# Kernel tuning notes

Hardware: AMD Instinct MI355X
Metric: run time of the kernel (lower is better)

## Reference

```python
import jax, jax.numpy as jnp
import numpy as np

B, L, QD, H, D = 2, 2048, 1024, 16, 64  # batch, seq, q_dim, heads, head_dim
INNER = H * D


def rms_norm(x, scale):
    # matches torch RMSNorm: mean over last dim in fp32, eps=1e-6, learned scale
    rrms = jax.lax.rsqrt(jnp.mean(x.astype(jnp.float32) ** 2, axis=-1, keepdims=True) + 1e-6)
    return (x * rrms).astype(x.dtype) * scale


def apply_rope(xq, xk, pe):
    # pe: [1,1,L,D//2,2,2] rotation-matrix pairs (FLUX-style)
    def rot(x):
        xs = x.reshape(*x.shape[:-1], D // 2, 1, 2)  # B H L D/2 1 2
        out = pe[..., 0] * xs[..., 0] + pe[..., 1] * xs[..., 1]  # B H L D/2 2
        return out.reshape(x.shape).astype(x.dtype)
    return rot(xq), rot(xk)


def setup_inputs() -> dict:
    key = jax.random.key(0)
    ks = jax.random.split(key, 6)
    s = 0.02
    return {
        "x": jax.random.normal(ks[0], (B, L, QD), jnp.float32),
        "pe": jax.random.normal(ks[1], (1, 1, L, D // 2, 2, 2), jnp.float32),
        "Wq": jax.random.normal(ks[2], (INNER, QD), jnp.float32) * s,
        "Wkv": jax.random.normal(ks[3], (2 * INNER, QD), jnp.float32) * s,
        "Wproj": jax.random.normal(ks[4], (QD, INNER), jnp.float32) * s,
        "bproj": jnp.zeros((QD,), jnp.float32),
        "q_scale": jnp.ones((D,), jnp.float32),
        "k_scale": jnp.ones((D,), jnp.float32),
    }


def reference(x, pe, Wq, Wkv, Wproj, bproj, q_scale, k_scale):
    # q/kv projections (self-attention: context = x)
    q = jnp.einsum('blc,ec->ble', x, Wq).reshape(B, L, H, D).transpose(0, 2, 1, 3)  # B H L D
    kv = jnp.einsum('blc,ec->ble', x, Wkv).reshape(B, L, 2, H, D)  # layout (K H D)
    k = kv[:, :, 0].transpose(0, 2, 1, 3)  # B H L D
    v = kv[:, :, 1].transpose(0, 2, 1, 3)  # B H L D
    # per-head QK RMSNorm
    q = rms_norm(q, q_scale)
    k = rms_norm(k, k_scale)
    # RoPE then scaled dot-product attention
    q, k = apply_rope(q, k, pe)
    scores = jnp.einsum('bhqd,bhkd->bhqk', q, k) / np.float32(np.sqrt(D))
    attn = jax.nn.softmax(scores, axis=-1)
    o = jnp.einsum('bhqk,bhkd->bhqd', attn, v)
    o = o.transpose(0, 2, 1, 3).reshape(B, L, INNER)  # B L (H D)
    return o @ Wproj.T + bproj
```

## Files before the change

kernel.cpp:

```cpp
#include <hip/hip_runtime.h>
#include <hip/hip_bf16.h>
#include <stdint.h>

#define BB 2
#define LL 2048
#define QDIM 1024
#define NH 16
#define HD 64

using bf16x8 = __attribute__((ext_vector_type(8))) __bf16;
using bf16x2 = __attribute__((ext_vector_type(2))) __bf16;
using bf16x4 = __attribute__((ext_vector_type(4))) __bf16;
using f32x4  = __attribute__((ext_vector_type(4))) float;
using u16x8  = __attribute__((ext_vector_type(8))) unsigned short;
using u32x2  = __attribute__((ext_vector_type(2))) uint32_t;

__device__ __forceinline__ unsigned short f2bf(float f) {
  return __builtin_bit_cast(unsigned short, (__bf16)f);
}
__device__ __forceinline__ float bf2f(unsigned short h) {
  uint32_t u = ((uint32_t)h) << 16;
  return __builtin_bit_cast(float, u);
}
__device__ __forceinline__ uint32_t pkbf2(float a, float b) {
  bf16x2 v = { (__bf16)a, (__bf16)b };
  return __builtin_bit_cast(uint32_t, v);
}

__device__ __forceinline__ void gload_lds16(const void* g, void* l) {
  __builtin_amdgcn_global_load_lds((__attribute__((address_space(1))) void*)g,
                                   (__attribute__((address_space(3))) void*)l,
                                   16, 0, 0);
}

__global__ __launch_bounds__(256) void k_cast_bf16(const float* __restrict__ in,
                                                   unsigned short* __restrict__ out, int n) {
  int i = (blockIdx.x * 256 + threadIdx.x) * 8;
  if (i >= n) return;
  float4 a = *reinterpret_cast<const float4*>(in + i);
  float4 b = *reinterpret_cast<const float4*>(in + i + 4);
  u16x8 o;
  o[0] = f2bf(a.x); o[1] = f2bf(a.y); o[2] = f2bf(a.z); o[3] = f2bf(a.w);
  o[4] = f2bf(b.x); o[5] = f2bf(b.y); o[6] = f2bf(b.z); o[7] = f2bf(b.w);
  *reinterpret_cast<u16x8*>(out + i) = o;
}

__global__ __launch_bounds__(256) void k_gemm_qkv(const unsigned short* __restrict__ A,
                                                  const unsigned short* __restrict__ Bw,
                                                  unsigned short* __restrict__ qk,
                                                  unsigned short* __restrict__ vT) {
  __shared__ unsigned short As[128 * 32];
  __shared__ unsigned short Bs[128 * 32];
  const int t = threadIdx.x;
  const int lane = t & 63, w = t >> 6;
  const int wm = w >> 1, wn = w & 1;
  const int g = lane >> 4, r16 = lane & 15;
  const size_t am0 = (size_t)blockIdx.x * 128;
  const size_t bn0 = (size_t)blockIdx.y * 128;
  const int K = 1024;

  f32x4 acc[4][4] = {};

  const int o0 = t * 16, row0 = o0 >> 6, cb0 = o0 & 63;
  const int o1 = 4096 + t * 16, row1 = o1 >> 6, cb1 = o1 & 63;

  for (int kb = 0; kb < K; kb += 32) {
    __syncthreads();
    gload_lds16(A  + (am0 + row0) * K + kb + (cb0 >> 1), (char*)As + o0);
    gload_lds16(A  + (am0 + row1) * K + kb + (cb1 >> 1), (char*)As + o1);
    gload_lds16(Bw + (bn0 + row0) * K + kb + (cb0 >> 1), (char*)Bs + o0);
    gload_lds16(Bw + (bn0 + row1) * K + kb + (cb1 >> 1), (char*)Bs + o1);
    __syncthreads();

    bf16x8 af[4], bfr[4];
#pragma unroll
    for (int i = 0; i < 4; ++i)
      af[i] = *reinterpret_cast<const bf16x8*>((const char*)As + (wm * 64 + i * 16 + r16) * 64 + g * 16);
#pragma unroll
    for (int j = 0; j < 4; ++j)
      bfr[j] = *reinterpret_cast<const bf16x8*>((const char*)Bs + (wn * 64 + j * 16 + r16) * 64 + g * 16);
#pragma unroll
    for (int i = 0; i < 4; ++i)
#pragma unroll
      for (int j = 0; j < 4; ++j)
        acc[i][j] = __builtin_amdgcn_mfma_f32_16x16x32_bf16(af[i], bfr[j], acc[i][j], 0, 0, 0);
  }

#pragma unroll
  for (int i = 0; i < 4; ++i)
#pragma unroll
    for (int j = 0; j < 4; ++j) {
      size_t row = am0 + wm * 64 + i * 16 + g * 4;
      int col = (int)bn0 + wn * 64 + j * 16 + r16;
      if (col < 2048) {
#pragma unroll
        for (int r = 0; r < 4; ++r) qk[(row + r) * 2048 + col] = f2bf(acc[i][j][r]);
      } else {
        int e = col - 2048, h = e >> 6, d = e & 63;
        int b = (int)(row >> 11), l2 = (int)(row & 2047);
        ushort4 pk;
        pk.x = f2bf(acc[i][j][0]); pk.y = f2bf(acc[i][j][1]);
        pk.z = f2bf(acc[i][j][2]); pk.w = f2bf(acc[i][j][3]);
        *reinterpret_cast<ushort4*>(vT + ((size_t)(b * 16 + h) * 64 + d) * 2048 + l2) = pk;
      }
    }
}

__global__ __launch_bounds__(256) void k_gemm_proj(const unsigned short* __restrict__ A,
                                                   const unsigned short* __restrict__ Bw,
                                                   float* __restrict__ Cf,
                                                   const float* __restrict__ bias) {
  __shared__ unsigned short As[64 * 32];
  __shared__ unsigned short Bs[128 * 32];
  const int t = threadIdx.x;
  const int lane = t & 63, w = t >> 6;
  const int wm = w >> 1, wn = w & 1;
  const int g = lane >> 4, r16 = lane & 15;
  const size_t am0 = (size_t)blockIdx.x * 64;
  const size_t bn0 = (size_t)blockIdx.y * 128;
  const int K = 1024;

  f32x4 acc[2][4] = {};

  const int oa = t * 16, rowa = oa >> 6, cba = oa & 63;
  const int ob0 = t * 16, rowb0 = ob0 >> 6, cbb0 = ob0 & 63;
  const int ob1 = 4096 + t * 16, rowb1 = ob1 >> 6, cbb1 = ob1 & 63;

  for (int kb = 0; kb < K; kb += 32) {
    __syncthreads();
    gload_lds16(A  + (am0 + rowa)  * K + kb + (cba  >> 1), (char*)As + oa);
    gload_lds16(Bw + (bn0 + rowb0) * K + kb + (cbb0 >> 1), (char*)Bs + ob0);
    gload_lds16(Bw + (bn0 + rowb1) * K + kb + (cbb1 >> 1), (char*)Bs + ob1);
    __syncthreads();

    bf16x8 af[2], bfr[4];
#pragma unroll
    for (int i = 0; i < 2; ++i)
      af[i] = *reinterpret_cast<const bf16x8*>((const char*)As + (wm * 32 + i * 16 + r16) * 64 + g * 16);
#pragma unroll
    for (int j = 0; j < 4; ++j)
      bfr[j] = *reinterpret_cast<const bf16x8*>((const char*)Bs + (wn * 64 + j * 16 + r16) * 64 + g * 16);
#pragma unroll
    for (int i = 0; i < 2; ++i)
#pragma unroll
      for (int j = 0; j < 4; ++j)
        acc[i][j] = __builtin_amdgcn_mfma_f32_16x16x32_bf16(af[i], bfr[j], acc[i][j], 0, 0, 0);
  }

#pragma unroll
  for (int i = 0; i < 2; ++i)
#pragma unroll
    for (int j = 0; j < 4; ++j) {
      size_t row = am0 + wm * 32 + i * 16 + g * 4;
      int col = (int)bn0 + wn * 64 + j * 16 + r16;
#pragma unroll
      for (int r = 0; r < 4; ++r) Cf[(row + r) * 1024 + col] = acc[i][j][r] + bias[col];
    }
}

__global__ __launch_bounds__(256) void k_norm_rope(unsigned short* __restrict__ qkbuf,
                                                   const float* __restrict__ pe,
                                                   const float* __restrict__ qs,
                                                   const float* __restrict__ ks) {
  const float S2 = 0.125f * 1.44269504f;
  const int row = blockIdx.x;
  const int l = row & (LL - 1);
  const int t = threadIdx.x, w = t >> 6, lane = t & 63;
  const int hgrp = lane >> 5, dp = lane & 31;
  const size_t base = (size_t)row * 2048;
  const float4 pev = *reinterpret_cast<const float4*>(pe + ((size_t)l * 32 + dp) * 4);
  const float2 qsv0 = *reinterpret_cast<const float2*>(qs + dp * 2);
  const float2 ksv = *reinterpret_cast<const float2*>(ks + dp * 2);
  const float2 qsv = { qsv0.x * S2, qsv0.y * S2 };

#pragma unroll
  for (int pass = 0; pass < 4; ++pass) {
    const int isK = pass >> 1;
    const int h = w * 4 + (pass & 1) * 2 + hgrp;
    unsigned short* p = qkbuf + base + isK * 1024 + h * 64 + dp * 2;
    uint32_t v = *reinterpret_cast<uint32_t*>(p);
    float xe = bf2f((unsigned short)(v & 0xffff)), xo = bf2f((unsigned short)(v >> 16));
    float s = xe * xe + xo * xo;
#pragma unroll
    for (int mk = 1; mk < 32; mk <<= 1) s += __shfl_xor(s, mk);
    float rr = rsqrtf(s * (1.0f / 64.0f) + 1e-6f);
    float sx = isK ? ksv.x : qsv.x, sy = isK ? ksv.y : qsv.y;
    float ne = xe * rr * sx, no = xo * rr * sy;
    float oe = pev.x * ne + pev.y * no;
    float oo = pev.z * ne + pev.w * no;
    *reinterpret_cast<uint32_t*>(p) = (uint32_t)f2bf(oe) | ((uint32_t)f2bf(oo) << 16);
  }
}

__global__ __launch_bounds__(256, 4) void k_flash(const unsigned short* __restrict__ qkbuf,
                                                  const unsigned short* __restrict__ vT,
                                                  unsigned short* __restrict__ ob) {
  __shared__ unsigned short Plds[4][16][64];
  __shared__ unsigned short Ktile[2][64 * 64];
  __shared__ unsigned short Vtile[2][64 * 64];
  const int t = threadIdx.x, w = t >> 6, lane = t & 63;
  const int g = lane >> 4, r16 = lane & 15;
  const int id = blockIdx.x;
  const int bh = (id & 7) + (((id >> 3) & 3) << 3);
  const int lt = id >> 5;
  const int b = bh >> 4, h = bh & 15;
  const int l0 = lt * 64 + w * 16;
  const size_t qkb = (size_t)b * LL * 2048;
  const unsigned short* Qp = qkbuf + qkb + (size_t)(l0 + r16) * 2048 + h * 64;
  const unsigned short* Kbase = qkbuf + qkb + 1024 + h * 64;
  const unsigned short* Vbase = vT + (size_t)bh * 64 * 2048;

  const bf16x8 qf0 = *reinterpret_cast<const bf16x8*>(Qp + g * 8);
  const bf16x8 qf1 = *reinterpret_cast<const bf16x8*>(Qp + 32 + g * 8);

  f32x4 oacc[4] = {};
  float m = -1e30f, lsum = 0.f;

  char* Pw = (char*)&Plds[w][0][0];
  const int pswz = (r16 & 7) << 4;
  const int prow = r16 * 128;
  const int wr0 = prow + ((0 * 32 + g * 8) ^ pswz);
  const int wr1 = prow + ((1 * 32 + g * 8) ^ pswz);
  const int wr2 = prow + ((2 * 32 + g * 8) ^ pswz);
  const int wr3 = prow + ((3 * 32 + g * 8) ^ pswz);
  const int rd0 = prow + ((g * 16) ^ pswz);
  const int rd1 = prow + ((64 + g * 16) ^ pswz);

  const int so0 = t * 16, sr0 = so0 >> 7, sl0 = (so0 & 127) ^ ((sr0 & 7) << 4);
  const int so1 = 4096 + t * 16, sr1 = so1 >> 7, sl1 = (so1 & 127) ^ ((sr1 & 7) << 4);

  gload_lds16(Kbase + (size_t)sr0 * 2048 + (sl0 >> 1), (char*)&Ktile[0][0] + so0);
  gload_lds16(Kbase + (size_t)sr1 * 2048 + (sl1 >> 1), (char*)&Ktile[0][0] + so1);
  gload_lds16(Vbase + (size_t)sr0 * 2048 + (sl0 >> 1), (char*)&Vtile[0][0] + so0);
  gload_lds16(Vbase + (size_t)sr1 * 2048 + (sl1 >> 1), (char*)&Vtile[0][0] + so1);
  __syncthreads();

  const int kswz = (r16 & 7) << 4;

  for (int kt = 0; kt < LL; kt += 64) {
    const int cur = (kt >> 6) & 1;
    if (kt + 64 < LL) {
      const int nxt = cur ^ 1;
      gload_lds16(Kbase + (size_t)(kt + 64 + sr0) * 2048 + (sl0 >> 1), (char*)&Ktile[nxt][0] + so0);
      gload_lds16(Kbase + (size_t)(kt + 64 + sr1) * 2048 + (sl1 >> 1), (char*)&Ktile[nxt][0] + so1);
      gload_lds16(Vbase + (size_t)sr0 * 2048 + kt + 64 + (sl0 >> 1), (char*)&Vtile[nxt][0] + so0);
      gload_lds16(Vbase + (size_t)sr1 * 2048 + kt + 64 + (sl1 >> 1), (char*)&Vtile[nxt][0] + so1);
    }
    const char* Kt = (const char*)&Ktile[cur][0];
    const char* Vt = (const char*)&Vtile[cur][0];

    f32x4 s[4];
#pragma unroll
    for (int kb = 0; kb < 4; ++kb) {
      const char* kp = Kt + (kb * 16 + r16) * 128;
      bf16x8 ka0 = *reinterpret_cast<const bf16x8*>(kp + ((g * 16) ^ kswz));
      bf16x8 ka1 = *reinterpret_cast<const bf16x8*>(kp + ((64 + g * 16) ^ kswz));
      f32x4 z = {};
      z = __builtin_amdgcn_mfma_f32_16x16x32_bf16(ka0, qf0, z, 0, 0, 0);
      z = __builtin_amdgcn_mfma_f32_16x16x32_bf16(ka1, qf1, z, 0, 0, 0);
      s[kb] = z;
    }
    float p[16];
#pragma unroll
    for (int kb = 0; kb < 4; ++kb)
#pragma unroll
      for (int r = 0; r < 4; ++r) p[kb * 4 + r] = s[kb][r];
    float tm = p[0];
#pragma unroll
    for (int i = 1; i < 16; ++i) tm = fmaxf(tm, p[i]);
    tm = fmaxf(tm, __shfl_xor(tm, 16));
    tm = fmaxf(tm, __shfl_xor(tm, 32));
    if (!__all(tm <= m + 11.0f)) {
      float nm = fmaxf(m, tm);
      float alpha = __builtin_exp2f(m - nm);
      lsum *= alpha;
#pragma unroll
      for (int dt = 0; dt < 4; ++dt) oacc[dt] *= alpha;
      m = nm;
    }
    float ts = 0.f;
#pragma unroll
    for (int i = 0; i < 16; ++i) { p[i] = __builtin_exp2f(p[i] - m); ts += p[i]; }
    ts += __shfl_xor(ts, 16);
    ts += __shfl_xor(ts, 32);
    lsum += ts;
    {
      u32x2 wv;
      wv[0] = pkbf2(p[0],  p[1]);  wv[1] = pkbf2(p[2],  p[3]);
      *reinterpret_cast<u32x2*>(Pw + wr0) = wv;
      wv[0] = pkbf2(p[4],  p[5]);  wv[1] = pkbf2(p[6],  p[7]);
      *reinterpret_cast<u32x2*>(Pw + wr1) = wv;
      wv[0] = pkbf2(p[8],  p[9]);  wv[1] = pkbf2(p[10], p[11]);
      *reinterpret_cast<u32x2*>(Pw + wr2) = wv;
      wv[0] = pkbf2(p[12], p[13]); wv[1] = pkbf2(p[14], p[15]);
      *reinterpret_cast<u32x2*>(Pw + wr3) = wv;
    }
    __asm__ __volatile__("s_waitcnt lgkmcnt(0)" ::: "memory");
    bf16x8 pb0 = *reinterpret_cast<const bf16x8*>(Pw + rd0);
    bf16x8 pb1 = *reinterpret_cast<const bf16x8*>(Pw + rd1);
#pragma unroll
    for (int dt = 0; dt < 4; ++dt) {
      const char* vp = Vt + (dt * 16 + r16) * 128;
      bf16x8 va0 = *reinterpret_cast<const bf16x8*>(vp + ((g * 16) ^ kswz));
      bf16x8 va1 = *reinterpret_cast<const bf16x8*>(vp + ((64 + g * 16) ^ kswz));
      oacc[dt] = __builtin_amdgcn_mfma_f32_16x16x32_bf16(va0, pb0, oacc[dt], 0, 0, 0);
      oacc[dt] = __builtin_amdgcn_mfma_f32_16x16x32_bf16(va1, pb1, oacc[dt], 0, 0, 0);
    }
    __syncthreads();
  }

  const float inv = 1.0f / lsum;
  const size_t orow = (size_t)(b * LL + l0 + r16) * 1024 + h * 64;
#pragma unroll
  for (int dt = 0; dt < 4; ++dt) {
    ushort4 pk;
    pk.x = f2bf(oacc[dt][0] * inv); pk.y = f2bf(oacc[dt][1] * inv);
    pk.z = f2bf(oacc[dt][2] * inv); pk.w = f2bf(oacc[dt][3] * inv);
    *reinterpret_cast<ushort4*>(ob + orow + dt * 16 + g * 4) = pk;
  }
}

extern "C" void kernel_launch(void* const* d_in, const int* in_sizes, int n_in,
                              void* d_out, int out_size, void* d_ws, size_t ws_size,
                              hipStream_t stream) {
  const float* x     = (const float*)d_in[0];
  const float* pe    = (const float*)d_in[1];
  const float* Wq    = (const float*)d_in[2];
  const float* Wkv   = (const float*)d_in[3];
  const float* Wproj = (const float*)d_in[4];
  const float* bproj = (const float*)d_in[5];
  const float* qs    = (const float*)d_in[6];
  const float* ks    = (const float*)d_in[7];
  float* out = (float*)d_out;

  char* ws = (char*)d_ws;
  unsigned short* xb     = (unsigned short*)(ws);
  unsigned short* Wall   = (unsigned short*)(ws + 8u  * 1024 * 1024);
  unsigned short* Wprojb = (unsigned short*)(ws + 14u * 1024 * 1024);
  unsigned short* qk     = (unsigned short*)(ws + 16u * 1024 * 1024);
  unsigned short* vT     = (unsigned short*)(ws + 32u * 1024 * 1024);
  unsigned short* ob     = (unsigned short*)(ws + 40u * 1024 * 1024);

  k_cast_bf16<<<4194304 / 2048, 256, 0, stream>>>(x, xb, 4194304);
  k_cast_bf16<<<1048576 / 2048, 256, 0, stream>>>(Wq, Wall, 1048576);
  k_cast_bf16<<<2097152 / 2048, 256, 0, stream>>>(Wkv, Wall + 1048576, 2097152);
  k_cast_bf16<<<1048576 / 2048, 256, 0, stream>>>(Wproj, Wprojb, 1048576);

  k_gemm_qkv<<<dim3(32, 24), 256, 0, stream>>>(xb, Wall, qk, vT);

  k_norm_rope<<<BB * LL, 256, 0, stream>>>(qk, pe, qs, ks);
  k_flash<<<1024, 256, 0, stream>>>(qk, vT, ob);

  k_gemm_proj<<<dim3(64, 8), 256, 0, stream>>>(ob, Wprojb, out, bproj);
}
```

Before: 227.5 us.

## Double-buffer GEMM LDS tiles and process two query tiles per flash wave

Both GEMM kernels now double-buffer their LDS tiles, issuing the next k-slice's async global-to-LDS loads before the current slice's MFMAs, which removes one barrier per iteration. The flash attention kernel gives each wave two 16-row query tiles 64 rows apart, so each K/V LDS tile feeds twice as many MFMAs. This halves the grid to 512 blocks and lowers the occupancy hint from 4 to 2. The max and sum reductions are rebalanced into trees. The cost is more registers and fewer resident blocks, which may leave fewer waves to hide latency.

```diff
diff --git a/kernel.cpp b/kernel.cpp
--- a/kernel.cpp
+++ b/kernel.cpp
@@ -10,7 +10,6 @@
 
 using bf16x8 = __attribute__((ext_vector_type(8))) __bf16;
 using bf16x2 = __attribute__((ext_vector_type(2))) __bf16;
-using bf16x4 = __attribute__((ext_vector_type(4))) __bf16;
 using f32x4  = __attribute__((ext_vector_type(4))) float;
 using u16x8  = __attribute__((ext_vector_type(8))) unsigned short;
 using u32x2  = __attribute__((ext_vector_type(2))) uint32_t;
@@ -49,8 +48,8 @@
                                                   const unsigned short* __restrict__ Bw,
                                                   unsigned short* __restrict__ qk,
                                                   unsigned short* __restrict__ vT) {
-  __shared__ unsigned short As[128 * 32];
-  __shared__ unsigned short Bs[128 * 32];
+  __shared__ unsigned short As[2][128 * 32];
+  __shared__ unsigned short Bs[2][128 * 32];
   const int t = threadIdx.x;
   const int lane = t & 63, w = t >> 6;
   const int wm = w >> 1, wn = w & 1;
@@ -64,26 +63,34 @@
   const int o0 = t * 16, row0 = o0 >> 6, cb0 = o0 & 63;
   const int o1 = 4096 + t * 16, row1 = o1 >> 6, cb1 = o1 & 63;
 
+  gload_lds16(A  + (am0 + row0) * K + (cb0 >> 1), (char*)&As[0][0] + o0);
+  gload_lds16(A  + (am0 + row1) * K + (cb1 >> 1), (char*)&As[0][0] + o1);
+  gload_lds16(Bw + (bn0 + row0) * K + (cb0 >> 1), (char*)&Bs[0][0] + o0);
+  gload_lds16(Bw + (bn0 + row1) * K + (cb1 >> 1), (char*)&Bs[0][0] + o1);
+  __syncthreads();
+
   for (int kb = 0; kb < K; kb += 32) {
-    __syncthreads();
-    gload_lds16(A  + (am0 + row0) * K + kb + (cb0 >> 1), (char*)As + o0);
-    gload_lds16(A  + (am0 + row1) * K + kb + (cb1 >> 1), (char*)As + o1);
-    gload_lds16(Bw + (bn0 + row0) * K + kb + (cb0 >> 1), (char*)Bs + o0);
-    gload_lds16(Bw + (bn0 + row1) * K + kb + (cb1 >> 1), (char*)Bs + o1);
-    __syncthreads();
-
+    const int cur = (kb >> 5) & 1;
+    if (kb + 32 < K) {
+      const int nxt = cur ^ 1;
+      gload_lds16(A  + (am0 + row0) * K + kb + 32 + (cb0 >> 1), (char*)&As[nxt][0] + o0);
+      gload_lds16(A  + (am0 + row1) * K + kb + 32 + (cb1 >> 1), (char*)&As[nxt][0] + o1);
+      gload_lds16(Bw + (bn0 + row0) * K + kb + 32 + (cb0 >> 1), (char*)&Bs[nxt][0] + o0);
+      gload_lds16(Bw + (bn0 + row1) * K + kb + 32 + (cb1 >> 1), (char*)&Bs[nxt][0] + o1);
+    }
     bf16x8 af[4], bfr[4];
 #pragma unroll
     for (int i = 0; i < 4; ++i)
-      af[i] = *reinterpret_cast<const bf16x8*>((const char*)As + (wm * 64 + i * 16 + r16) * 64 + g * 16);
+      af[i] = *reinterpret_cast<const bf16x8*>((const char*)&As[cur][0] + (wm * 64 + i * 16 + r16) * 64 + g * 16);
 #pragma unroll
     for (int j = 0; j < 4; ++j)
-      bfr[j] = *reinterpret_cast<const bf16x8*>((const char*)Bs + (wn * 64 + j * 16 + r16) * 64 + g * 16);
+      bfr[j] = *reinterpret_cast<const bf16x8*>((const char*)&Bs[cur][0] + (wn * 64 + j * 16 + r16) * 64 + g * 16);
 #pragma unroll
     for (int i = 0; i < 4; ++i)
 #pragma unroll
       for (int j = 0; j < 4; ++j)
         acc[i][j] = __builtin_amdgcn_mfma_f32_16x16x32_bf16(af[i], bfr[j], acc[i][j], 0, 0, 0);
+    __syncthreads();
   }
 
 #pragma unroll
@@ -110,8 +117,8 @@
                                                    const unsigned short* __restrict__ Bw,
                                                    float* __restrict__ Cf,
                                                    const float* __restrict__ bias) {
-  __shared__ unsigned short As[64 * 32];
-  __shared__ unsigned short Bs[128 * 32];
+  __shared__ unsigned short As[2][64 * 32];
+  __shared__ unsigned short Bs[2][128 * 32];
   const int t = threadIdx.x;
   const int lane = t & 63, w = t >> 6;
   const int wm = w >> 1, wn = w & 1;
@@ -126,25 +133,32 @@
   const int ob0 = t * 16, rowb0 = ob0 >> 6, cbb0 = ob0 & 63;
   const int ob1 = 4096 + t * 16, rowb1 = ob1 >> 6, cbb1 = ob1 & 63;
 
+  gload_lds16(A  + (am0 + rowa)  * K + (cba  >> 1), (char*)&As[0][0] + oa);
+  gload_lds16(Bw + (bn0 + rowb0) * K + (cbb0 >> 1), (char*)&Bs[0][0] + ob0);
+  gload_lds16(Bw + (bn0 + rowb1) * K + (cbb1 >> 1), (char*)&Bs[0][0] + ob1);
+  __syncthreads();
+
   for (int kb = 0; kb < K; kb += 32) {
-    __syncthreads();
-    gload_lds16(A  + (am0 + rowa)  * K + kb + (cba  >> 1), (char*)As + oa);
-    gload_lds16(Bw + (bn0 + rowb0) * K + kb + (cbb0 >> 1), (char*)Bs + ob0);
-    gload_lds16(Bw + (bn0 + rowb1) * K + kb + (cbb1 >> 1), (char*)Bs + ob1);
-    __syncthreads();
-
+    const int cur = (kb >> 5) & 1;
+    if (kb + 32 < K) {
+      const int nxt = cur ^ 1;
+      gload_lds16(A  + (am0 + rowa)  * K + kb + 32 + (cba  >> 1), (char*)&As[nxt][0] + oa);
+      gload_lds16(Bw + (bn0 + rowb0) * K + kb + 32 + (cbb0 >> 1), (char*)&Bs[nxt][0] + ob0);
+      gload_lds16(Bw + (bn0 + rowb1) * K + kb + 32 + (cbb1 >> 1), (char*)&Bs[nxt][0] + ob1);
+    }
     bf16x8 af[2], bfr[4];
 #pragma unroll
     for (int i = 0; i < 2; ++i)
-      af[i] = *reinterpret_cast<const bf16x8*>((const char*)As + (wm * 32 + i * 16 + r16) * 64 + g * 16);
+      af[i] = *reinterpret_cast<const bf16x8*>((const char*)&As[cur][0] + (wm * 32 + i * 16 + r16) * 64 + g * 16);
 #pragma unroll
     for (int j = 0; j < 4; ++j)
-      bfr[j] = *reinterpret_cast<const bf16x8*>((const char*)Bs + (wn * 64 + j * 16 + r16) * 64 + g * 16);
+      bfr[j] = *reinterpret_cast<const bf16x8*>((const char*)&Bs[cur][0] + (wn * 64 + j * 16 + r16) * 64 + g * 16);
 #pragma unroll
     for (int i = 0; i < 2; ++i)
 #pragma unroll
       for (int j = 0; j < 4; ++j)
         acc[i][j] = __builtin_amdgcn_mfma_f32_16x16x32_bf16(af[i], bfr[j], acc[i][j], 0, 0, 0);
+    __syncthreads();
   }
 
 #pragma unroll
@@ -192,31 +206,35 @@
   }
 }
 
-__global__ __launch_bounds__(256, 4) void k_flash(const unsigned short* __restrict__ qkbuf,
+__global__ __launch_bounds__(256, 2) void k_flash(const unsigned short* __restrict__ qkbuf,
                                                   const unsigned short* __restrict__ vT,
                                                   unsigned short* __restrict__ ob) {
-  __shared__ unsigned short Plds[4][16][64];
   __shared__ unsigned short Ktile[2][64 * 64];
   __shared__ unsigned short Vtile[2][64 * 64];
+  __shared__ unsigned short Plds[4][2][16 * 64];
   const int t = threadIdx.x, w = t >> 6, lane = t & 63;
   const int g = lane >> 4, r16 = lane & 15;
   const int id = blockIdx.x;
   const int bh = (id & 7) + (((id >> 3) & 3) << 3);
   const int lt = id >> 5;
   const int b = bh >> 4, h = bh & 15;
-  const int l0 = lt * 64 + w * 16;
+  const int l0 = lt * 128 + w * 16;
   const size_t qkb = (size_t)b * LL * 2048;
   const unsigned short* Qp = qkbuf + qkb + (size_t)(l0 + r16) * 2048 + h * 64;
   const unsigned short* Kbase = qkbuf + qkb + 1024 + h * 64;
   const unsigned short* Vbase = vT + (size_t)bh * 64 * 2048;
 
-  const bf16x8 qf0 = *reinterpret_cast<const bf16x8*>(Qp + g * 8);
-  const bf16x8 qf1 = *reinterpret_cast<const bf16x8*>(Qp + 32 + g * 8);
-
-  f32x4 oacc[4] = {};
-  float m = -1e30f, lsum = 0.f;
-
-  char* Pw = (char*)&Plds[w][0][0];
+  bf16x8 qf[2][2];
+  qf[0][0] = *reinterpret_cast<const bf16x8*>(Qp + g * 8);
+  qf[0][1] = *reinterpret_cast<const bf16x8*>(Qp + 32 + g * 8);
+  qf[1][0] = *reinterpret_cast<const bf16x8*>(Qp + (size_t)64 * 2048 + g * 8);
+  qf[1][1] = *reinterpret_cast<const bf16x8*>(Qp + (size_t)64 * 2048 + 32 + g * 8);
+
+  f32x4 oacc[2][4] = {};
+  float m[2] = {-1e30f, -1e30f}, lsum[2] = {0.f, 0.f};
+
+  char* Pw0 = (char*)&Plds[w][0][0];
+  char* Pw1 = (char*)&Plds[w][1][0];
   const int pswz = (r16 & 7) << 4;
   const int prow = r16 * 128;
   const int wr0 = prow + ((0 * 32 + g * 8) ^ pswz);
@@ -249,42 +267,54 @@
     const char* Kt = (const char*)&Ktile[cur][0];
     const char* Vt = (const char*)&Vtile[cur][0];
 
-    f32x4 s[4];
+    f32x4 s[2][4];
 #pragma unroll
     for (int kb = 0; kb < 4; ++kb) {
       const char* kp = Kt + (kb * 16 + r16) * 128;
       bf16x8 ka0 = *reinterpret_cast<const bf16x8*>(kp + ((g * 16) ^ kswz));
       bf16x8 ka1 = *reinterpret_cast<const bf16x8*>(kp + ((64 + g * 16) ^ kswz));
-      f32x4 z = {};
-      z = __builtin_amdgcn_mfma_f32_16x16x32_bf16(ka0, qf0, z, 0, 0, 0);
-      z = __builtin_amdgcn_mfma_f32_16x16x32_bf16(ka1, qf1, z, 0, 0, 0);
-      s[kb] = z;
-    }
-    float p[16];
-#pragma unroll
-    for (int kb = 0; kb < 4; ++kb)
-#pragma unroll
-      for (int r = 0; r < 4; ++r) p[kb * 4 + r] = s[kb][r];
-    float tm = p[0];
-#pragma unroll
-    for (int i = 1; i < 16; ++i) tm = fmaxf(tm, p[i]);
-    tm = fmaxf(tm, __shfl_xor(tm, 16));
-    tm = fmaxf(tm, __shfl_xor(tm, 32));
-    if (!__all(tm <= m + 11.0f)) {
-      float nm = fmaxf(m, tm);
-      float alpha = __builtin_exp2f(m - nm);
-      lsum *= alpha;
-#pragma unroll
-      for (int dt = 0; dt < 4; ++dt) oacc[dt] *= alpha;
-      m = nm;
-    }
-    float ts = 0.f;
-#pragma unroll
-    for (int i = 0; i < 16; ++i) { p[i] = __builtin_exp2f(p[i] - m); ts += p[i]; }
-    ts += __shfl_xor(ts, 16);
-    ts += __shfl_xor(ts, 32);
-    lsum += ts;
-    {
+#pragma unroll
+      for (int j = 0; j < 2; ++j) {
+        f32x4 z = {};
+        z = __builtin_amdgcn_mfma_f32_16x16x32_bf16(ka0, qf[j][0], z, 0, 0, 0);
+        z = __builtin_amdgcn_mfma_f32_16x16x32_bf16(ka1, qf[j][1], z, 0, 0, 0);
+        s[j][kb] = z;
+      }
+    }
+#pragma unroll
+    for (int j = 0; j < 2; ++j) {
+      float p[16];
+#pragma unroll
+      for (int kb = 0; kb < 4; ++kb)
+#pragma unroll
+        for (int r = 0; r < 4; ++r) p[kb * 4 + r] = s[j][kb][r];
+      float t0 = fmaxf(fmaxf(p[0], p[1]), p[2]);
+      float t1 = fmaxf(fmaxf(p[3], p[4]), p[5]);
+      float t2 = fmaxf(fmaxf(p[6], p[7]), p[8]);
+      float t3 = fmaxf(fmaxf(p[9], p[10]), p[11]);
+      float t4 = fmaxf(fmaxf(p[12], p[13]), p[14]);
+      float tm = fmaxf(fmaxf(fmaxf(t0, t1), t2), fmaxf(fmaxf(t3, t4), p[15]));
+      tm = fmaxf(tm, __shfl_xor(tm, 16));
+      tm = fmaxf(tm, __shfl_xor(tm, 32));
+      if (!__all(tm <= m[j] + 11.0f)) {
+        float nm = fmaxf(m[j], tm);
+        float alpha = __builtin_exp2f(m[j] - nm);
+        lsum[j] *= alpha;
+#pragma unroll
+        for (int dt = 0; dt < 4; ++dt) oacc[j][dt] *= alpha;
+        m[j] = nm;
+      }
+#pragma unroll
+      for (int i = 0; i < 16; ++i) p[i] = __builtin_exp2f(p[i] - m[j]);
+      float a0 = (p[0] + p[1]) + (p[2] + p[3]);
+      float a1 = (p[4] + p[5]) + (p[6] + p[7]);
+      float a2 = (p[8] + p[9]) + (p[10] + p[11]);
+      float a3 = (p[12] + p[13]) + (p[14] + p[15]);
+      float ts = (a0 + a1) + (a2 + a3);
+      ts += __shfl_xor(ts, 16);
+      ts += __shfl_xor(ts, 32);
+      lsum[j] += ts;
+      char* Pw = j ? Pw1 : Pw0;
       u32x2 wv;
       wv[0] = pkbf2(p[0],  p[1]);  wv[1] = pkbf2(p[2],  p[3]);
       *reinterpret_cast<u32x2*>(Pw + wr0) = wv;
@@ -296,27 +326,36 @@
       *reinterpret_cast<u32x2*>(Pw + wr3) = wv;
     }
     __asm__ __volatile__("s_waitcnt lgkmcnt(0)" ::: "memory");
-    bf16x8 pb0 = *reinterpret_cast<const bf16x8*>(Pw + rd0);
-    bf16x8 pb1 = *reinterpret_cast<const bf16x8*>(Pw + rd1);
+    bf16x8 pb[2][2];
+    pb[0][0] = *reinterpret_cast<const bf16x8*>(Pw0 + rd0);
+    pb[0][1] = *reinterpret_cast<const bf16x8*>(Pw0 + rd1);
+    pb[1][0] = *reinterpret_cast<const bf16x8*>(Pw1 + rd0);
+    pb[1][1] = *reinterpret_cast<const bf16x8*>(Pw1 + rd1);
 #pragma unroll
     for (int dt = 0; dt < 4; ++dt) {
       const char* vp = Vt + (dt * 16 + r16) * 128;
       bf16x8 va0 = *reinterpret_cast<const bf16x8*>(vp + ((g * 16) ^ kswz));
       bf16x8 va1 = *reinterpret_cast<const bf16x8*>(vp + ((64 + g * 16) ^ kswz));
-      oacc[dt] = __builtin_amdgcn_mfma_f32_16x16x32_bf16(va0, pb0, oacc[dt], 0, 0, 0);
-      oacc[dt] = __builtin_amdgcn_mfma_f32_16x16x32_bf16(va1, pb1, oacc[dt], 0, 0, 0);
+#pragma unroll
+      for (int j = 0; j < 2; ++j) {
+        oacc[j][dt] = __builtin_amdgcn_mfma_f32_16x16x32_bf16(va0, pb[j][0], oacc[j][dt], 0, 0, 0);
+        oacc[j][dt] = __builtin_amdgcn_mfma_f32_16x16x32_bf16(va1, pb[j][1], oacc[j][dt], 0, 0, 0);
+      }
     }
     __syncthreads();
   }
 
-  const float inv = 1.0f / lsum;
-  const size_t orow = (size_t)(b * LL + l0 + r16) * 1024 + h * 64;
-#pragma unroll
-  for (int dt = 0; dt < 4; ++dt) {
-    ushort4 pk;
-    pk.x = f2bf(oacc[dt][0] * inv); pk.y = f2bf(oacc[dt][1] * inv);
-    pk.z = f2bf(oacc[dt][2] * inv); pk.w = f2bf(oacc[dt][3] * inv);
-    *reinterpret_cast<ushort4*>(ob + orow + dt * 16 + g * 4) = pk;
+#pragma unroll
+  for (int j = 0; j < 2; ++j) {
+    const float inv = 1.0f / lsum[j];
+    const size_t orow = (size_t)(b * LL + l0 + j * 64 + r16) * 1024 + h * 64;
+#pragma unroll
+    for (int dt = 0; dt < 4; ++dt) {
+      ushort4 pk;
+      pk.x = f2bf(oacc[j][dt][0] * inv); pk.y = f2bf(oacc[j][dt][1] * inv);
+      pk.z = f2bf(oacc[j][dt][2] * inv); pk.w = f2bf(oacc[j][dt][3] * inv);
+      *reinterpret_cast<ushort4*>(ob + orow + dt * 16 + g * 4) = pk;
+    }
   }
 }
 
@@ -349,7 +388,7 @@
   k_gemm_qkv<<<dim3(32, 24), 256, 0, stream>>>(xb, Wall, qk, vT);
 
   k_norm_rope<<<BB * LL, 256, 0, stream>>>(qk, pe, qs, ks);
-  k_flash<<<1024, 256, 0, stream>>>(qk, vT, ob);
+  k_flash<<<512, 256, 0, stream>>>(qk, vT, ob);
 
   k_gemm_proj<<<dim3(64, 8), 256, 0, stream>>>(ob, Wprojb, out, bproj);
 }
```

After: 236.5 us. +4.0%, slower.
